# Optimization experiments

Hardware: AMD Instinct MI355X
Metric: run time of the kernel (lower is better)

Reference implementation:

```python
import jax, jax.numpy as jnp
import numpy as np

B, N, C, H = 2, 384, 256, 4
D = C // H


def setup_inputs() -> dict:
    key = jax.random.key(0)
    k1, k2 = jax.random.split(key)
    x = jax.random.normal(k1, (B, N, C), dtype=jnp.float32)
    # nn.Linear(dim, 8*dim, bias=False) weight, scaled like default torch init magnitude
    W = jax.random.normal(k2, (8 * C, C), dtype=jnp.float32) / np.float32(np.sqrt(C))
    return {"x": x, "W": W}


def reference(x, W):
    Bx, Nx, Cx = x.shape
    Hh = H
    Dd = Cx // Hh
    scale = Dd ** -0.5
    # w(x): [B,N,8C] -> [B,N,8,H,D] -> [8,B,H,N,D]
    w = (x @ W.T).reshape(Bx, Nx, 8, Hh, Dd).transpose(2, 0, 3, 1, 4)
    a, b, c = w[0], w[1], w[2]          # w[3..5] (d,e,f) are unused in the torch forward
    v1, v2 = w[6], w[7]
    # pairwise logits, each [B,H,N,N]
    eAB = jnp.exp(jnp.einsum('bhid,bhjd->bhij', a, b) * scale)  # indexed [i,j]
    eCD = jnp.exp(jnp.einsum('bhid,bhjd->bhij', b, c) * scale)  # indexed [i,k]
    eEF = jnp.exp(jnp.einsum('bhid,bhjd->bhij', c, a) * scale)  # indexed [j,k]
    # exact factorization of exp(AB[ij]+CD[ik]+EF[jk]):
    # num[i,d] = sum_j eAB[ij] v1[jd] * (sum_k eCD[ik] eEF[jk] v2[kd])
    T = eEF[..., None] * v2[:, :, None, :, :]                   # [B,H,j,k,D]
    R = jnp.einsum('bhik,bhjkd->bhijd', eCD, T)                 # [B,H,i,j,D]
    num = jnp.einsum('bhij,bhjd,bhijd->bhid', eAB, v1, R)       # [B,H,N,D]
    den = jnp.sum(eAB * jnp.einsum('bhik,bhjk->bhij', eCD, eEF), axis=-1)  # [B,H,N]
    out = num / den[..., None]
    # [B,H,N,D] -> [B,N,H,D] -> [B,N,C]
    return out.transpose(0, 2, 1, 3).reshape(Bx, Nx, Cx)
```

## Files before the change

kernel.cpp:

```cpp
#include <hip/hip_runtime.h>
#include <math.h>

#define B_  2
#define N_  384
#define C_  256
#define H_  4
#define D_  64
#define NBH (B_*H_)
#define TSZ (NBH*N_*D_)
#define ESZ (NBH*N_*N_)
#define SCALE 0.125f
#define PIT 72

typedef _Float16 f16;
typedef f16  f16x8 __attribute__((ext_vector_type(8)));
typedef f16  f16x4 __attribute__((ext_vector_type(4)));
typedef float f32x4 __attribute__((ext_vector_type(4)));

__global__ __launch_bounds__(256) void proj_kernel(const float* __restrict__ x,
                                                   const float* __restrict__ W,
                                                   float* __restrict__ proj) {
    __shared__ float Xs[32][68];
    __shared__ float Ws[32][68];
    const int tid = threadIdx.x;
    const int tx = tid & 15, ty = tid >> 4;
    const int m0 = blockIdx.x * 64;
    const int c0 = blockIdx.y * 64;
    const int t  = c0 >> 8;
    const int wbase = ((t >= 3) ? (t + 3) : t) * 256;

    float acc[4][4] = {{0.f}};
    for (int k0 = 0; k0 < 256; k0 += 32) {
        __syncthreads();
#pragma unroll
        for (int l = 0; l < 8; ++l) {
            const int idx = l * 256 + tid;
            const int mi = idx >> 5, kk = idx & 31;
            Xs[kk][mi] = x[(m0 + mi) * 256 + k0 + kk];
            const int rem = (c0 + mi) & 255;
            Ws[kk][mi] = W[(wbase + rem) * 256 + k0 + kk];
        }
        __syncthreads();
#pragma unroll
        for (int kk = 0; kk < 32; ++kk) {
            const float4 xf = *(const float4*)&Xs[kk][ty * 4];
            const float4 wf = *(const float4*)&Ws[kk][tx * 4];
            const float xa[4] = {xf.x, xf.y, xf.z, xf.w};
            const float wa[4] = {wf.x, wf.y, wf.z, wf.w};
#pragma unroll
            for (int q = 0; q < 4; ++q)
#pragma unroll
                for (int p = 0; p < 4; ++p)
                    acc[q][p] += xa[q] * wa[p];
        }
    }
#pragma unroll
    for (int q = 0; q < 4; ++q) {
        const int r = m0 + ty * 4 + q;
        const int b = r / N_;
        const int n = r - b * N_;
#pragma unroll
        for (int p = 0; p < 4; ++p) {
            const int rem = (c0 + tx * 4 + p) & 255;
            const int h = rem >> 6, d = rem & 63;
            proj[t * TSZ + ((b * H_ + h) * N_ + n) * D_ + d] = acc[q][p];
        }
    }
}

__global__ __launch_bounds__(256) void logits_kernel(const float* __restrict__ proj,
                                                     f16* __restrict__ eabt16,
                                                     float* __restrict__ ecd,
                                                     f16* __restrict__ eef16) {
    __shared__ float Xs[32][68];
    __shared__ float Ys[32][68];
    const int tid = threadIdx.x;
    const int tx = tid & 15, ty = tid >> 4;
    const int i0 = blockIdx.x * 64, j0 = blockIdx.y * 64;
    const int q  = blockIdx.z >> 3;
    const int bh = blockIdx.z & 7;
    const int xt = q;
    const int yt = (q == 2) ? 0 : (q + 1);
    const float* Xp = proj + xt * TSZ + bh * N_ * D_;
    const float* Yp = proj + yt * TSZ + bh * N_ * D_;

    float acc[4][4] = {{0.f}};
    for (int k0 = 0; k0 < 64; k0 += 32) {
        __syncthreads();
#pragma unroll
        for (int l = 0; l < 8; ++l) {
            const int idx = l * 256 + tid;
            const int mi = idx >> 5, kk = idx & 31;
            Xs[kk][mi] = Xp[(i0 + mi) * 64 + k0 + kk];
            Ys[kk][mi] = Yp[(j0 + mi) * 64 + k0 + kk];
        }
        __syncthreads();
#pragma unroll
        for (int kk = 0; kk < 32; ++kk) {
            const float4 xf = *(const float4*)&Xs[kk][ty * 4];
            const float4 yf = *(const float4*)&Ys[kk][tx * 4];
            const float xa[4] = {xf.x, xf.y, xf.z, xf.w};
            const float ya[4] = {yf.x, yf.y, yf.z, yf.w};
#pragma unroll
            for (int qq = 0; qq < 4; ++qq)
#pragma unroll
                for (int p = 0; p < 4; ++p)
                    acc[qq][p] += xa[qq] * ya[p];
        }
    }
#pragma unroll
    for (int qq = 0; qq < 4; ++qq)
#pragma unroll
        for (int p = 0; p < 4; ++p) {
            const float e = expf(acc[qq][p] * SCALE);
            const int ii = i0 + ty * 4 + qq;
            const int jj = j0 + tx * 4 + p;
            if (q == 0)      eabt16[(size_t)bh * N_ * N_ + jj * N_ + ii] = (f16)e;
            else if (q == 1) ecd   [(size_t)bh * N_ * N_ + ii * N_ + jj] = e;
            else             eef16 [(size_t)bh * N_ * N_ + ii * N_ + jj] = (f16)e;
        }
}

__global__ __launch_bounds__(256) void triplet_mfma_kernel(
        const f16*  __restrict__ eabt,
        const float* __restrict__ ecd,
        const f16*  __restrict__ eef,
        const float* __restrict__ v1,
        const float* __restrict__ v2,
        float* __restrict__ numout) {
    __shared__ __align__(16) unsigned char smem_raw[62464];
    f16*   us   = (f16*)smem_raw;
    f16*   es   = us + 4 * 64 * PIT;
    f16*   abts = es + 64 * PIT;
    float* v1s  = (float*)(smem_raw + 55296);
    float* v2k  = (float*)(smem_raw + 61440);

    const int tid  = threadIdx.x;
    const int lane = tid & 63;
    const int w    = tid >> 6;
    const int quad = lane >> 4;
    const int lr   = lane & 15;
    const int i0 = blockIdx.x * 64;
    const int dg = blockIdx.y;
    const int bh = blockIdx.z;
    const int dd = dg * 4 + w;

    const f16*   eabtb = eabt + (size_t)bh * N_ * N_;
    const float* ecdb  = ecd  + (size_t)bh * N_ * N_;
    const f16*   eefb  = eef  + (size_t)bh * N_ * N_;
    const float* v1b   = v1 + (size_t)bh * N_ * D_;
    const float* v2b   = v2 + (size_t)bh * N_ * D_;

#pragma unroll
    for (int it = 0; it < 6; ++it) {
        const int id = it * 256 + tid;
        const int j = id >> 2, c = id & 3;
        const int d2 = dg * 4 + c;
        v1s[id] = (d2 < 64) ? v1b[j * 64 + d2] : 1.0f;
    }

    float numacc[16];
#pragma unroll
    for (int r = 0; r < 16; ++r) numacc[r] = 0.f;

    for (int kt = 0; kt < 6; ++kt) {
        const int k0 = kt * 64;
        __syncthreads();
        {
            const int c = tid >> 6, k = tid & 63;
            const int d2 = dg * 4 + c;
            v2k[c * 64 + k] = (d2 < 64) ? v2b[(k0 + k) * 64 + d2] : 1.0f;
        }
        __syncthreads();
#pragma unroll
        for (int it = 0; it < 4; ++it) {
            const int row  = it * 16 + (tid >> 4);
            const int kcol = (tid & 15) * 4;
            const float4 c4 = *(const float4*)&ecdb[(i0 + row) * N_ + k0 + kcol];
#pragma unroll
            for (int d = 0; d < 4; ++d) {
                const float4 w4 = *(const float4*)&v2k[d * 64 + kcol];
                union { f16 h[4]; unsigned long long u; } pk;
                pk.h[0] = (f16)(c4.x * w4.x);
                pk.h[1] = (f16)(c4.y * w4.y);
                pk.h[2] = (f16)(c4.z * w4.z);
                pk.h[3] = (f16)(c4.w * w4.w);
                *(unsigned long long*)(us + d * 64 * PIT + row * PIT + kcol) = pk.u;
            }
        }
        __syncthreads();
        f16x8 af[4][2];
#pragma unroll
        for (int isub = 0; isub < 4; ++isub)
#pragma unroll
            for (int ks = 0; ks < 2; ++ks)
                af[isub][ks] = *(const f16x8*)(us + w * 64 * PIT +
                                               (isub * 16 + lr) * PIT + (ks * 4 + quad) * 8);

        for (int jt = 0; jt < 6; ++jt) {
            const int j0 = jt * 64;
            __syncthreads();
#pragma unroll
            for (int it = 0; it < 2; ++it) {
                const int row = it * 32 + (tid >> 3);
                const int blk = tid & 7;
                *(uint4*)(es   + row * PIT + blk * 8) =
                    *(const uint4*)(eefb  + (j0 + row) * N_ + k0 + blk * 8);
                *(uint4*)(abts + row * PIT + blk * 8) =
                    *(const uint4*)(eabtb + (j0 + row) * N_ + i0 + blk * 8);
            }
            __syncthreads();
            f16x8 bf[4][2];
#pragma unroll
            for (int js = 0; js < 4; ++js)
#pragma unroll
                for (int ks = 0; ks < 2; ++ks)
                    bf[js][ks] = *(const f16x8*)(es + (js * 16 + lr) * PIT + (ks * 4 + quad) * 8);
#pragma unroll
            for (int js = 0; js < 4; ++js) {
                const float v1v = v1s[(j0 + js * 16 + lr) * 4 + w];
#pragma unroll
                for (int isub = 0; isub < 4; ++isub) {
                    f32x4 t = {0.f, 0.f, 0.f, 0.f};
                    t = __builtin_amdgcn_mfma_f32_16x16x32_f16(af[isub][0], bf[js][0], t, 0, 0, 0);
                    t = __builtin_amdgcn_mfma_f32_16x16x32_f16(af[isub][1], bf[js][1], t, 0, 0, 0);
                    const f16x4 ab = *(const f16x4*)(abts + (js * 16 + lr) * PIT +
                                                     isub * 16 + quad * 4);
#pragma unroll
                    for (int q = 0; q < 4; ++q)
                        numacc[isub * 4 + q] += (float)ab[q] * (v1v * t[q]);
                }
            }
        }
    }
#pragma unroll
    for (int r = 0; r < 16; ++r) {
        float v = numacc[r];
        v += __shfl_xor(v, 1);
        v += __shfl_xor(v, 2);
        v += __shfl_xor(v, 4);
        v += __shfl_xor(v, 8);
        numacc[r] = v;
    }
    if (lr == 0) {
#pragma unroll
        for (int r = 0; r < 16; ++r) {
            const int i = (r >> 2) * 16 + quad * 4 + (r & 3);
            numout[((size_t)bh * N_ + i0 + i) * 68 + dd] = numacc[r];
        }
    }
}

__global__ __launch_bounds__(256) void finalize_kernel(const float* __restrict__ numw,
                                                       float* __restrict__ out) {
    const int o = blockIdx.x * 256 + threadIdx.x;
    const int b = o / (N_ * C_);
    const int rem = o - b * (N_ * C_);
    const int n = rem >> 8;
    const int cc = rem & 255;
    const int h = cc >> 6, d = cc & 63;
    const float* base = numw + (((size_t)b * H_ + h) * N_ + n) * 68;
    out[o] = base[d] / base[64];
}

extern "C" void kernel_launch(void* const* d_in, const int* in_sizes, int n_in,
                              void* d_out, int out_size, void* d_ws, size_t ws_size,
                              hipStream_t stream) {
    const float* x = (const float*)d_in[0];
    const float* W = (const float*)d_in[1];
    float* ws    = (float*)d_ws;
    float* proj  = ws;
    float* ecd   = ws + 5 * TSZ;
    float* numw  = ecd + ESZ;
    f16*   eabt  = (f16*)(numw + NBH * N_ * 68);
    f16*   eef   = eabt + ESZ;

    proj_kernel<<<dim3(12, 20), 256, 0, stream>>>(x, W, proj);
    logits_kernel<<<dim3(6, 6, 24), 256, 0, stream>>>(proj, eabt, ecd, eef);
    triplet_mfma_kernel<<<dim3(6, 17, 8), 256, 0, stream>>>(
        eabt, ecd, eef, proj + 3 * TSZ, proj + 4 * TSZ, numw);
    finalize_kernel<<<dim3(768), 256, 0, stream>>>(numw, (float*)d_out);
}
```

Measured before the change: 252.2 us.

## Split triplet kernel over k halves and build A fragments in registers

The triplet kernel's k loop is split into two halves, each handled by its own block, which doubles the grid. Each half writes a separate partial numerator/denominator buffer, and the finalize kernel adds the two before dividing. The eCD·v2 A fragments are now computed straight into registers from global memory instead of being staged through shared memory. That cuts LDS use from about 62KB to 25KB and removes one barrier, and a launch_bounds hint of 4 blocks per multiprocessor is added to raise occupancy. The cost is an extra partial buffer (reusing the dead projection workspace), redundant eAB/eEF tile loads across the two splits, and possible register pressure.

```diff
diff --git a/kernel.cpp b/kernel.cpp
--- a/kernel.cpp
+++ b/kernel.cpp
@@ -11,6 +11,7 @@
 #define ESZ (NBH*N_*N_)
 #define SCALE 0.125f
 #define PIT 72
+#define NWSLICE (NBH*N_*68)
 
 typedef _Float16 f16;
 typedef f16  f16x8 __attribute__((ext_vector_type(8)));
@@ -121,19 +122,19 @@
         }
 }
 
-__global__ __launch_bounds__(256) void triplet_mfma_kernel(
+__global__ __launch_bounds__(256, 4) void triplet_mfma_kernel(
         const f16*  __restrict__ eabt,
         const float* __restrict__ ecd,
         const f16*  __restrict__ eef,
         const float* __restrict__ v1,
         const float* __restrict__ v2,
-        float* __restrict__ numout) {
-    __shared__ __align__(16) unsigned char smem_raw[62464];
-    f16*   us   = (f16*)smem_raw;
-    f16*   es   = us + 4 * 64 * PIT;
+        float* __restrict__ num0,
+        float* __restrict__ num1) {
+    __shared__ __align__(16) unsigned char smem_raw[25600];
+    f16*   es   = (f16*)smem_raw;
     f16*   abts = es + 64 * PIT;
-    float* v1s  = (float*)(smem_raw + 55296);
-    float* v2k  = (float*)(smem_raw + 61440);
+    float* v1s  = (float*)(smem_raw + 18432);
+    float* v2k  = (float*)(smem_raw + 24576);
 
     const int tid  = threadIdx.x;
     const int lane = tid & 63;
@@ -142,7 +143,9 @@
     const int lr   = lane & 15;
     const int i0 = blockIdx.x * 64;
     const int dg = blockIdx.y;
-    const int bh = blockIdx.z;
+    const int zz = blockIdx.z;
+    const int bh    = zz & 7;
+    const int split = zz >> 3;
     const int dd = dg * 4 + w;
 
     const f16*   eabtb = eabt + (size_t)bh * N_ * N_;
@@ -150,6 +153,7 @@
     const f16*   eefb  = eef  + (size_t)bh * N_ * N_;
     const float* v1b   = v1 + (size_t)bh * N_ * D_;
     const float* v2b   = v2 + (size_t)bh * N_ * D_;
+    float* numout = split ? num1 : num0;
 
 #pragma unroll
     for (int it = 0; it < 6; ++it) {
@@ -163,7 +167,8 @@
 #pragma unroll
     for (int r = 0; r < 16; ++r) numacc[r] = 0.f;
 
-    for (int kt = 0; kt < 6; ++kt) {
+    const int ktbeg = split * 3;
+    for (int kt = ktbeg; kt < ktbeg + 3; ++kt) {
         const int k0 = kt * 64;
         __syncthreads();
         {
@@ -172,30 +177,32 @@
             v2k[c * 64 + k] = (d2 < 64) ? v2b[(k0 + k) * 64 + d2] : 1.0f;
         }
         __syncthreads();
-#pragma unroll
-        for (int it = 0; it < 4; ++it) {
-            const int row  = it * 16 + (tid >> 4);
-            const int kcol = (tid & 15) * 4;
-            const float4 c4 = *(const float4*)&ecdb[(i0 + row) * N_ + k0 + kcol];
-#pragma unroll
-            for (int d = 0; d < 4; ++d) {
-                const float4 w4 = *(const float4*)&v2k[d * 64 + kcol];
-                union { f16 h[4]; unsigned long long u; } pk;
-                pk.h[0] = (f16)(c4.x * w4.x);
-                pk.h[1] = (f16)(c4.y * w4.y);
-                pk.h[2] = (f16)(c4.z * w4.z);
-                pk.h[3] = (f16)(c4.w * w4.w);
-                *(unsigned long long*)(us + d * 64 * PIT + row * PIT + kcol) = pk.u;
+        float4 v2a[2][2];
+#pragma unroll
+        for (int ks = 0; ks < 2; ++ks) {
+            v2a[ks][0] = *(const float4*)&v2k[w * 64 + ks * 32 + quad * 8];
+            v2a[ks][1] = *(const float4*)&v2k[w * 64 + ks * 32 + quad * 8 + 4];
+        }
+        f16x8 af[4][2];
+#pragma unroll
+        for (int isub = 0; isub < 4; ++isub) {
+            const float* rowp = ecdb + (i0 + isub * 16 + lr) * N_ + k0 + quad * 8;
+#pragma unroll
+            for (int ks = 0; ks < 2; ++ks) {
+                const float4 c0 = *(const float4*)(rowp + ks * 32);
+                const float4 c1 = *(const float4*)(rowp + ks * 32 + 4);
+                union { f16 h[8]; f16x8 v; } pk;
+                pk.h[0] = (f16)(c0.x * v2a[ks][0].x);
+                pk.h[1] = (f16)(c0.y * v2a[ks][0].y);
+                pk.h[2] = (f16)(c0.z * v2a[ks][0].z);
+                pk.h[3] = (f16)(c0.w * v2a[ks][0].w);
+                pk.h[4] = (f16)(c1.x * v2a[ks][1].x);
+                pk.h[5] = (f16)(c1.y * v2a[ks][1].y);
+                pk.h[6] = (f16)(c1.z * v2a[ks][1].z);
+                pk.h[7] = (f16)(c1.w * v2a[ks][1].w);
+                af[isub][ks] = pk.v;
             }
         }
-        __syncthreads();
-        f16x8 af[4][2];
-#pragma unroll
-        for (int isub = 0; isub < 4; ++isub)
-#pragma unroll
-            for (int ks = 0; ks < 2; ++ks)
-                af[isub][ks] = *(const f16x8*)(us + w * 64 * PIT +
-                                               (isub * 16 + lr) * PIT + (ks * 4 + quad) * 8);
 
         for (int jt = 0; jt < 6; ++jt) {
             const int j0 = jt * 64;
@@ -251,7 +258,8 @@
     }
 }
 
-__global__ __launch_bounds__(256) void finalize_kernel(const float* __restrict__ numw,
+__global__ __launch_bounds__(256) void finalize_kernel(const float* __restrict__ num0,
+                                                       const float* __restrict__ num1,
                                                        float* __restrict__ out) {
     const int o = blockIdx.x * 256 + threadIdx.x;
     const int b = o / (N_ * C_);
@@ -259,8 +267,10 @@
     const int n = rem >> 8;
     const int cc = rem & 255;
     const int h = cc >> 6, d = cc & 63;
-    const float* base = numw + (((size_t)b * H_ + h) * N_ + n) * 68;
-    out[o] = base[d] / base[64];
+    const size_t base = (((size_t)b * H_ + h) * N_ + n) * 68;
+    const float nmr = num0[base + d]  + num1[base + d];
+    const float dnr = num0[base + 64] + num1[base + 64];
+    out[o] = nmr / dnr;
 }
 
 extern "C" void kernel_launch(void* const* d_in, const int* in_sizes, int n_in,
@@ -271,13 +281,14 @@
     float* ws    = (float*)d_ws;
     float* proj  = ws;
     float* ecd   = ws + 5 * TSZ;
-    float* numw  = ecd + ESZ;
-    f16*   eabt  = (f16*)(numw + NBH * N_ * 68);
+    float* num1  = ecd + ESZ;
+    f16*   eabt  = (f16*)(num1 + NWSLICE);
     f16*   eef   = eabt + ESZ;
+    float* num0  = ws;
 
     proj_kernel<<<dim3(12, 20), 256, 0, stream>>>(x, W, proj);
     logits_kernel<<<dim3(6, 6, 24), 256, 0, stream>>>(proj, eabt, ecd, eef);
-    triplet_mfma_kernel<<<dim3(6, 17, 8), 256, 0, stream>>>(
-        eabt, ecd, eef, proj + 3 * TSZ, proj + 4 * TSZ, numw);
-    finalize_kernel<<<dim3(768), 256, 0, stream>>>(numw, (float*)d_out);
-}
+    triplet_mfma_kernel<<<dim3(6, 17, 16), 256, 0, stream>>>(
+        eabt, ecd, eef, proj + 3 * TSZ, proj + 4 * TSZ, num0, num1);
+    finalize_kernel<<<dim3(768), 256, 0, stream>>>(num0, num1, (float*)d_out);
+}
```

Measured after the change: 521.9 us. 107% more time.

## Double-buffer eEF/eAB tiles with register prefetch in triplet MFMA kernel

Applied to the files above, without the earlier changes.

Splits the eEF and eAB^T shared-memory tiles into two buffers. Each next j-tile is loaded into registers before the MFMA work on the current tile and written to the other buffer afterward, so global latency overlaps compute and one barrier per j iteration is removed. This raises LDS use from about 61KB to about 79KB per block, which can lower occupancy, and adds live registers for the prefetched values.

```diff
diff --git a/kernel.cpp b/kernel.cpp
--- a/kernel.cpp
+++ b/kernel.cpp
@@ -128,12 +128,12 @@
         const float* __restrict__ v1,
         const float* __restrict__ v2,
         float* __restrict__ numout) {
-    __shared__ __align__(16) unsigned char smem_raw[62464];
+    __shared__ __align__(16) unsigned char smem_raw[80896];
     f16*   us   = (f16*)smem_raw;
-    f16*   es   = us + 4 * 64 * PIT;
-    f16*   abts = es + 64 * PIT;
-    float* v1s  = (float*)(smem_raw + 55296);
-    float* v2k  = (float*)(smem_raw + 61440);
+    f16*   es2  = (f16*)(smem_raw + 36864);
+    f16*   ab2  = (f16*)(smem_raw + 55296);
+    float* v1s  = (float*)(smem_raw + 73728);
+    float* v2k  = (float*)(smem_raw + 79872);
 
     const int tid  = threadIdx.x;
     const int lane = tid & 63;
@@ -158,24 +158,34 @@
         const int d2 = dg * 4 + c;
         v1s[id] = (d2 < 64) ? v1b[j * 64 + d2] : 1.0f;
     }
+    __syncthreads();
 
     float numacc[16];
 #pragma unroll
     for (int r = 0; r < 16; ++r) numacc[r] = 0.f;
+
+    const f32x4 zero4 = {0.f, 0.f, 0.f, 0.f};
+
+    const int brow = tid >> 4;
+    const int kcol = (tid & 15) * 4;
+    const int srow = tid >> 3;
+    const int sblk = tid & 7;
 
     for (int kt = 0; kt < 6; ++kt) {
         const int k0 = kt * 64;
-        __syncthreads();
         {
             const int c = tid >> 6, k = tid & 63;
             const int d2 = dg * 4 + c;
             v2k[c * 64 + k] = (d2 < 64) ? v2b[(k0 + k) * 64 + d2] : 1.0f;
         }
         __syncthreads();
+        uint4 pe0 = *(const uint4*)(eefb  + srow        * N_ + k0 + sblk * 8);
+        uint4 pe1 = *(const uint4*)(eefb  + (32 + srow) * N_ + k0 + sblk * 8);
+        uint4 pa0 = *(const uint4*)(eabtb + srow        * N_ + i0 + sblk * 8);
+        uint4 pa1 = *(const uint4*)(eabtb + (32 + srow) * N_ + i0 + sblk * 8);
 #pragma unroll
         for (int it = 0; it < 4; ++it) {
-            const int row  = it * 16 + (tid >> 4);
-            const int kcol = (tid & 15) * 4;
+            const int row = it * 16 + brow;
             const float4 c4 = *(const float4*)&ecdb[(i0 + row) * N_ + k0 + kcol];
 #pragma unroll
             for (int d = 0; d < 4; ++d) {
@@ -188,6 +198,10 @@
                 *(unsigned long long*)(us + d * 64 * PIT + row * PIT + kcol) = pk.u;
             }
         }
+        *(uint4*)(es2 + srow * PIT + sblk * 8)        = pe0;
+        *(uint4*)(es2 + (32 + srow) * PIT + sblk * 8) = pe1;
+        *(uint4*)(ab2 + srow * PIT + sblk * 8)        = pa0;
+        *(uint4*)(ab2 + (32 + srow) * PIT + sblk * 8) = pa1;
         __syncthreads();
         f16x8 af[4][2];
 #pragma unroll
@@ -199,38 +213,43 @@
 
         for (int jt = 0; jt < 6; ++jt) {
             const int j0 = jt * 64;
-            __syncthreads();
-#pragma unroll
-            for (int it = 0; it < 2; ++it) {
-                const int row = it * 32 + (tid >> 3);
-                const int blk = tid & 7;
-                *(uint4*)(es   + row * PIT + blk * 8) =
-                    *(const uint4*)(eefb  + (j0 + row) * N_ + k0 + blk * 8);
-                *(uint4*)(abts + row * PIT + blk * 8) =
-                    *(const uint4*)(eabtb + (j0 + row) * N_ + i0 + blk * 8);
+            const int p  = jt & 1;
+            const f16* esp = es2 + p * 64 * PIT;
+            const f16* abp = ab2 + p * 64 * PIT;
+            uint4 qe0, qe1, qa0, qa1;
+            if (jt < 5) {
+                const int jn = j0 + 64;
+                qe0 = *(const uint4*)(eefb  + (jn + srow)      * N_ + k0 + sblk * 8);
+                qe1 = *(const uint4*)(eefb  + (jn + 32 + srow) * N_ + k0 + sblk * 8);
+                qa0 = *(const uint4*)(eabtb + (jn + srow)      * N_ + i0 + sblk * 8);
+                qa1 = *(const uint4*)(eabtb + (jn + 32 + srow) * N_ + i0 + sblk * 8);
             }
-            __syncthreads();
-            f16x8 bf[4][2];
-#pragma unroll
-            for (int js = 0; js < 4; ++js)
-#pragma unroll
-                for (int ks = 0; ks < 2; ++ks)
-                    bf[js][ks] = *(const f16x8*)(es + (js * 16 + lr) * PIT + (ks * 4 + quad) * 8);
 #pragma unroll
             for (int js = 0; js < 4; ++js) {
+                const f16x8 bf0 = *(const f16x8*)(esp + (js * 16 + lr) * PIT + quad * 8);
+                const f16x8 bf1 = *(const f16x8*)(esp + (js * 16 + lr) * PIT + (4 + quad) * 8);
                 const float v1v = v1s[(j0 + js * 16 + lr) * 4 + w];
 #pragma unroll
                 for (int isub = 0; isub < 4; ++isub) {
-                    f32x4 t = {0.f, 0.f, 0.f, 0.f};
-                    t = __builtin_amdgcn_mfma_f32_16x16x32_f16(af[isub][0], bf[js][0], t, 0, 0, 0);
-                    t = __builtin_amdgcn_mfma_f32_16x16x32_f16(af[isub][1], bf[js][1], t, 0, 0, 0);
-                    const f16x4 ab = *(const f16x4*)(abts + (js * 16 + lr) * PIT +
+                    f32x4 t;
+                    t = __builtin_amdgcn_mfma_f32_16x16x32_f16(af[isub][0], bf0, zero4, 0, 0, 0);
+                    t = __builtin_amdgcn_mfma_f32_16x16x32_f16(af[isub][1], bf1, t, 0, 0, 0);
+                    const f16x4 ab = *(const f16x4*)(abp + (js * 16 + lr) * PIT +
                                                      isub * 16 + quad * 4);
 #pragma unroll
                     for (int q = 0; q < 4; ++q)
                         numacc[isub * 4 + q] += (float)ab[q] * (v1v * t[q]);
                 }
             }
+            if (jt < 5) {
+                f16* esn = es2 + (p ^ 1) * 64 * PIT;
+                f16* abn = ab2 + (p ^ 1) * 64 * PIT;
+                *(uint4*)(esn + srow * PIT + sblk * 8)        = qe0;
+                *(uint4*)(esn + (32 + srow) * PIT + sblk * 8) = qe1;
+                *(uint4*)(abn + srow * PIT + sblk * 8)        = qa0;
+                *(uint4*)(abn + (32 + srow) * PIT + sblk * 8) = qa1;
+            }
+            __syncthreads();
         }
     }
 #pragma unroll
```

Result: slower. 259.8 us (+3.0%).

## Halve triplet kernel i-tile, swizzle LDS layout, and stream v1 per j-tile

Applied to the files above, without the earlier changes.

The triplet MFMA kernel now handles 32 query rows per block instead of 64, so its grid doubles along x. It replaces the padded LDS layout with an XOR-swizzled 128-byte-row layout and loads v1 per j-tile instead of all at once. Together these cut shared memory from about 62KB to 34KB, meant to allow more resident blocks per CU and avoid bank conflicts without padding. In exchange, each block re-reads the eEF tiles and the full 64-column eAB tile while using only half of the latter. The last i-block also reads past the row end into adjacent buffer memory.

```diff
diff --git a/kernel.cpp b/kernel.cpp
--- a/kernel.cpp
+++ b/kernel.cpp
@@ -10,7 +10,6 @@
 #define TSZ (NBH*N_*D_)
 #define ESZ (NBH*N_*N_)
 #define SCALE 0.125f
-#define PIT 72
 
 typedef _Float16 f16;
 typedef f16  f16x8 __attribute__((ext_vector_type(8)));
@@ -128,19 +127,16 @@
         const float* __restrict__ v1,
         const float* __restrict__ v2,
         float* __restrict__ numout) {
-    __shared__ __align__(16) unsigned char smem_raw[62464];
-    f16*   us   = (f16*)smem_raw;
-    f16*   es   = us + 4 * 64 * PIT;
-    f16*   abts = es + 64 * PIT;
-    float* v1s  = (float*)(smem_raw + 55296);
-    float* v2k  = (float*)(smem_raw + 61440);
+    __shared__ __align__(16) unsigned char smem[34816];
+    float* v1t = (float*)(smem + 32768);
+    float* v2k = (float*)(smem + 33792);
 
     const int tid  = threadIdx.x;
     const int lane = tid & 63;
     const int w    = tid >> 6;
     const int quad = lane >> 4;
     const int lr   = lane & 15;
-    const int i0 = blockIdx.x * 64;
+    const int i0 = blockIdx.x * 32;
     const int dg = blockIdx.y;
     const int bh = blockIdx.z;
     const int dd = dg * 4 + w;
@@ -151,17 +147,17 @@
     const float* v1b   = v1 + (size_t)bh * N_ * D_;
     const float* v2b   = v2 + (size_t)bh * N_ * D_;
 
-#pragma unroll
-    for (int it = 0; it < 6; ++it) {
-        const int id = it * 256 + tid;
-        const int j = id >> 2, c = id & 3;
-        const int d2 = dg * 4 + c;
-        v1s[id] = (d2 < 64) ? v1b[j * 64 + d2] : 1.0f;
-    }
-
-    float numacc[16];
-#pragma unroll
-    for (int r = 0; r < 16; ++r) numacc[r] = 0.f;
+    float numacc[8];
+#pragma unroll
+    for (int r = 0; r < 8; ++r) numacc[r] = 0.f;
+
+    const f32x4 zero4 = {0.f, 0.f, 0.f, 0.f};
+
+    const int brow = tid >> 4;
+    const int tx   = tid & 15;
+    const int srow = tid >> 3;
+    const int sblk = tid & 7;
+    const int sw   = (lr & 7) << 4;
 
     for (int kt = 0; kt < 6; ++kt) {
         const int k0 = kt * 64;
@@ -173,59 +169,64 @@
         }
         __syncthreads();
 #pragma unroll
-        for (int it = 0; it < 4; ++it) {
-            const int row  = it * 16 + (tid >> 4);
-            const int kcol = (tid & 15) * 4;
-            const float4 c4 = *(const float4*)&ecdb[(i0 + row) * N_ + k0 + kcol];
+        for (int it = 0; it < 2; ++it) {
+            const int row = it * 16 + brow;
+            const float4 c4 = *(const float4*)&ecdb[(i0 + row) * N_ + k0 + tx * 4];
+            const int rowoff = (row * 128 + tx * 8) ^ ((row & 7) << 4);
 #pragma unroll
             for (int d = 0; d < 4; ++d) {
-                const float4 w4 = *(const float4*)&v2k[d * 64 + kcol];
+                const float4 w4 = *(const float4*)&v2k[d * 64 + tx * 4];
                 union { f16 h[4]; unsigned long long u; } pk;
                 pk.h[0] = (f16)(c4.x * w4.x);
                 pk.h[1] = (f16)(c4.y * w4.y);
                 pk.h[2] = (f16)(c4.z * w4.z);
                 pk.h[3] = (f16)(c4.w * w4.w);
-                *(unsigned long long*)(us + d * 64 * PIT + row * PIT + kcol) = pk.u;
-            }
-        }
-        __syncthreads();
-        f16x8 af[4][2];
-#pragma unroll
-        for (int isub = 0; isub < 4; ++isub)
+                *(unsigned long long*)(smem + d * 4096 + rowoff) = pk.u;
+            }
+        }
+        __syncthreads();
+        f16x8 af[2][2];
+#pragma unroll
+        for (int isub = 0; isub < 2; ++isub) {
+            const int row = isub * 16 + lr;
 #pragma unroll
             for (int ks = 0; ks < 2; ++ks)
-                af[isub][ks] = *(const f16x8*)(us + w * 64 * PIT +
-                                               (isub * 16 + lr) * PIT + (ks * 4 + quad) * 8);
+                af[isub][ks] = *(const f16x8*)(smem + w * 4096 + row * 128 +
+                                               (((ks * 4 + quad) * 16) ^ sw));
+        }
 
         for (int jt = 0; jt < 6; ++jt) {
             const int j0 = jt * 64;
             __syncthreads();
 #pragma unroll
             for (int it = 0; it < 2; ++it) {
-                const int row = it * 32 + (tid >> 3);
-                const int blk = tid & 7;
-                *(uint4*)(es   + row * PIT + blk * 8) =
-                    *(const uint4*)(eefb  + (j0 + row) * N_ + k0 + blk * 8);
-                *(uint4*)(abts + row * PIT + blk * 8) =
-                    *(const uint4*)(eabtb + (j0 + row) * N_ + i0 + blk * 8);
+                const int row = it * 32 + srow;
+                const int off = (row * 128 + sblk * 16) ^ ((row & 7) << 4);
+                *(uint4*)(smem + 16384 + off) =
+                    *(const uint4*)(eefb  + (j0 + row) * N_ + k0 + sblk * 8);
+                *(uint4*)(smem + 24576 + off) =
+                    *(const uint4*)(eabtb + (j0 + row) * N_ + i0 + sblk * 8);
+            }
+            {
+                const int j = tid >> 2, c = tid & 3;
+                const int d2 = dg * 4 + c;
+                v1t[tid] = (d2 < 64) ? v1b[(j0 + j) * 64 + d2] : 1.0f;
             }
             __syncthreads();
-            f16x8 bf[4][2];
-#pragma unroll
-            for (int js = 0; js < 4; ++js)
-#pragma unroll
-                for (int ks = 0; ks < 2; ++ks)
-                    bf[js][ks] = *(const f16x8*)(es + (js * 16 + lr) * PIT + (ks * 4 + quad) * 8);
 #pragma unroll
             for (int js = 0; js < 4; ++js) {
-                const float v1v = v1s[(j0 + js * 16 + lr) * 4 + w];
-#pragma unroll
-                for (int isub = 0; isub < 4; ++isub) {
-                    f32x4 t = {0.f, 0.f, 0.f, 0.f};
-                    t = __builtin_amdgcn_mfma_f32_16x16x32_f16(af[isub][0], bf[js][0], t, 0, 0, 0);
-                    t = __builtin_amdgcn_mfma_f32_16x16x32_f16(af[isub][1], bf[js][1], t, 0, 0, 0);
-                    const f16x4 ab = *(const f16x4*)(abts + (js * 16 + lr) * PIT +
-                                                     isub * 16 + quad * 4);
+                const int row = js * 16 + lr;
+                const int ro  = row * 128;
+                const f16x8 bf0 = *(const f16x8*)(smem + 16384 + ro + ((quad * 16) ^ sw));
+                const f16x8 bf1 = *(const f16x8*)(smem + 16384 + ro + (((4 + quad) * 16) ^ sw));
+                const float v1v = v1t[row * 4 + w];
+#pragma unroll
+                for (int isub = 0; isub < 2; ++isub) {
+                    f32x4 t;
+                    t = __builtin_amdgcn_mfma_f32_16x16x32_f16(af[isub][0], bf0, zero4, 0, 0, 0);
+                    t = __builtin_amdgcn_mfma_f32_16x16x32_f16(af[isub][1], bf1, t, 0, 0, 0);
+                    const f16x4 ab = *(const f16x4*)(smem + 24576 + ro +
+                                                     ((isub * 32 + quad * 8) ^ sw));
 #pragma unroll
                     for (int q = 0; q < 4; ++q)
                         numacc[isub * 4 + q] += (float)ab[q] * (v1v * t[q]);
@@ -234,7 +235,7 @@
         }
     }
 #pragma unroll
-    for (int r = 0; r < 16; ++r) {
+    for (int r = 0; r < 8; ++r) {
         float v = numacc[r];
         v += __shfl_xor(v, 1);
         v += __shfl_xor(v, 2);
@@ -244,7 +245,7 @@
     }
     if (lr == 0) {
 #pragma unroll
-        for (int r = 0; r < 16; ++r) {
+        for (int r = 0; r < 8; ++r) {
             const int i = (r >> 2) * 16 + quad * 4 + (r & 3);
             numout[((size_t)bh * N_ + i0 + i) * 68 + dd] = numacc[r];
         }
@@ -277,7 +278,7 @@
 
     proj_kernel<<<dim3(12, 20), 256, 0, stream>>>(x, W, proj);
     logits_kernel<<<dim3(6, 6, 24), 256, 0, stream>>>(proj, eabt, ecd, eef);
-    triplet_mfma_kernel<<<dim3(6, 17, 8), 256, 0, stream>>>(
+    triplet_mfma_kernel<<<dim3(12, 17, 8), 256, 0, stream>>>(
         eabt, ecd, eef, proj + 3 * TSZ, proj + 4 * TSZ, numw);
     finalize_kernel<<<dim3(768), 256, 0, stream>>>(numw, (float*)d_out);
 }
```

New measurement: 342.1 us. +35.6%, slower.
